# Kernel optimization log

Measured on AMD Instinct MI355X. Metric: run time of the kernel, lower is better.

## Reference

```python
import jax, jax.numpy as jnp
import numpy as np

N_ENT = 50000
N_REL = 500
N_EDGE = 800000
H_DIM = 96
BN_EPS = 1e-5


def setup_inputs() -> dict:
    key = jax.random.key(0)
    k1, k2, k3, k4, k5 = jax.random.split(key, 5)
    return {
        "ent_emb": jax.random.normal(k1, (N_ENT, H_DIM), dtype=jnp.float32),
        "rel_emb": jax.random.normal(k2, (N_REL, H_DIM), dtype=jnp.float32),
        "neigh_w": jax.random.normal(k3, (H_DIM, H_DIM), dtype=jnp.float32) * (1.0 / np.sqrt(H_DIM)),
        "bn_gamma": jnp.ones((H_DIM,), dtype=jnp.float32),
        "bn_beta": jnp.zeros((H_DIM,), dtype=jnp.float32),
        "rel_id": jax.random.randint(k4, (N_EDGE,), 0, N_REL, dtype=jnp.int64),
        "dst": jax.random.randint(k5, (N_EDGE,), 0, N_ENT, dtype=jnp.int64),
    }


def reference(ent_emb, rel_emb, neigh_w, bn_gamma, bn_beta, rel_id, dst):
    n_nodes = ent_emb.shape[0]
    # per-edge gather: edge feature = relation embedding  [E, D]
    e = rel_emb[rel_id]
    # e_dot_v: dot of edge feature with destination node embedding  [E]
    score = jnp.sum(e * ent_emb[dst], axis=-1)
    # edge softmax over incoming edges of each destination node
    seg_max = jax.ops.segment_max(score, dst, num_segments=n_nodes)  # [N]
    w = jnp.exp(score - seg_max[dst])                                # [E]
    seg_sum = jax.ops.segment_sum(w, dst, num_segments=n_nodes)      # [N]
    alpha = w / seg_sum[dst]                                         # [E]
    # weighted scatter-sum aggregation into destination nodes  [N, D]
    neigh = jax.ops.segment_sum(e * alpha[:, None], dst, num_segments=n_nodes)
    # linear
    out = neigh @ neigh_w
    # BatchNorm1d (training mode: batch stats over nodes, biased var)
    mu = jnp.mean(out, axis=0)
    var = jnp.mean((out - mu) ** 2, axis=0)
    out = (out - mu) * jax.lax.rsqrt(var + BN_EPS) * bn_gamma + bn_beta
    return jnp.tanh(out)
```

## Files before the change

### kernel.cpp

```cpp
#include <hip/hip_runtime.h>
#include <math.h>

#define N_ENT   50000
#define N_REL   500
#define N_EDGE  800000
#define H       96
#define BN_EPS  1e-5f
#define DEG_CAP 64

#define RELW_BLOCKS ((N_REL * H + 255) / 256)
#define ZERO_N      (N_ENT + 2 * H)
#define ZERO_BLOCKS ((ZERO_N + 255) / 256)

__global__ __launch_bounds__(256) void k_init(
        const float* __restrict__ rel, const float* __restrict__ W,
        float* __restrict__ relW, unsigned* __restrict__ zbase) {
    if (blockIdx.x < RELW_BLOCKS) {
        __shared__ float Ws[H * H];
        for (int i = threadIdx.x; i < H * H; i += 256) Ws[i] = W[i];
        __syncthreads();
        int t = blockIdx.x * 256 + threadIdx.x;
        if (t >= N_REL * H) return;
        int r = t / H;
        int c = t - r * H;
        const float4* rr = (const float4*)(rel + (size_t)r * H);
        float acc = 0.0f;
#pragma unroll
        for (int i = 0; i < H / 4; ++i) {
            float4 a = rr[i];
            acc += a.x * Ws[(4 * i + 0) * H + c];
            acc += a.y * Ws[(4 * i + 1) * H + c];
            acc += a.z * Ws[(4 * i + 2) * H + c];
            acc += a.w * Ws[(4 * i + 3) * H + c];
        }
        relW[t] = acc;
    } else {
        int i = (blockIdx.x - RELW_BLOCKS) * 256 + threadIdx.x;
        if (i < ZERO_N) zbase[i] = 0u;
    }
}

__global__ __launch_bounds__(256) void k_bucket(
        const int* __restrict__ dst, const int* __restrict__ rel_id,
        int* __restrict__ cursor, unsigned short* __restrict__ pay) {
    int e = blockIdx.x * 256 + threadIdx.x;
    if (e >= N_EDGE) return;
    int d = dst[e];
    int r = rel_id[e];
    int p = atomicAdd(cursor + d, 1);
    if (p < DEG_CAP) pay[d * DEG_CAP + p] = (unsigned short)r;
}

__global__ __launch_bounds__(256) void k_node(
        const float* __restrict__ ent, const float* __restrict__ rel,
        const unsigned short* __restrict__ pay, const int* __restrict__ cursor,
        const float* __restrict__ relW, float* __restrict__ out) {
    __shared__ float sh_w[4][DEG_CAP];
    __shared__ int   sh_r[4][DEG_CAP];
    int wv   = threadIdx.x >> 6;
    int lane = threadIdx.x & 63;
    int n = blockIdx.x * 4 + wv;
    if (n >= N_ENT) return;
    int cnt = min(cursor[n], DEG_CAP);

    {
        int q  = lane & 3;
        int jj = lane >> 2;
        const float4* er = (const float4*)(ent + (size_t)n * H) + q * 6;
        float4 e0 = er[0], e1 = er[1], e2 = er[2], e3 = er[3], e4 = er[4], e5 = er[5];
        int npass = (cnt + 15) >> 4;
        for (int p = 0; p < npass; ++p) {
            int j = (p << 4) + jj;
            bool valid = (j < cnt);
            int rid = valid ? (int)pay[n * DEG_CAP + j] : 0;
            float part = 0.0f;
            if (valid) {
                const float4* rr = (const float4*)(rel + (size_t)rid * H) + q * 6;
                float4 b;
                b = rr[0]; part += e0.x*b.x + e0.y*b.y + e0.z*b.z + e0.w*b.w;
                b = rr[1]; part += e1.x*b.x + e1.y*b.y + e1.z*b.z + e1.w*b.w;
                b = rr[2]; part += e2.x*b.x + e2.y*b.y + e2.z*b.z + e2.w*b.w;
                b = rr[3]; part += e3.x*b.x + e3.y*b.y + e3.z*b.z + e3.w*b.w;
                b = rr[4]; part += e4.x*b.x + e4.y*b.y + e4.z*b.z + e4.w*b.w;
                b = rr[5]; part += e5.x*b.x + e5.y*b.y + e5.z*b.z + e5.w*b.w;
            }
            part += __shfl_xor(part, 1);
            part += __shfl_xor(part, 2);
            if (valid && q == 0) { sh_w[wv][j] = part; sh_r[wv][j] = rid; }
        }
    }

    {
        float sc = (lane < cnt) ? sh_w[wv][lane] : -INFINITY;
        float m = sc;
#pragma unroll
        for (int off = 1; off < 64; off <<= 1)
            m = fmaxf(m, __shfl_xor(m, off));
        float w = (lane < cnt) ? __expf(sc - m) : 0.0f;
        float s = w;
#pragma unroll
        for (int off = 1; off < 64; off <<= 1)
            s += __shfl_xor(s, off);
        float inv = (cnt > 0) ? 1.0f / s : 0.0f;
        if (lane < cnt) sh_w[wv][lane] = w * inv;
    }

    int g  = lane & 7;
    int es = lane >> 3;
    float4 a0 = make_float4(0.f, 0.f, 0.f, 0.f);
    float4 a1 = make_float4(0.f, 0.f, 0.f, 0.f);
    float4 a2 = make_float4(0.f, 0.f, 0.f, 0.f);
    for (int k = es; k < cnt; k += 8) {
        float w  = sh_w[wv][k];
        int rid  = sh_r[wv][k];
        const float4* p = (const float4*)(relW + (size_t)rid * H + g * 12);
        float4 f0 = p[0], f1 = p[1], f2 = p[2];
        a0.x += w * f0.x; a0.y += w * f0.y; a0.z += w * f0.z; a0.w += w * f0.w;
        a1.x += w * f1.x; a1.y += w * f1.y; a1.z += w * f1.z; a1.w += w * f1.w;
        a2.x += w * f2.x; a2.y += w * f2.y; a2.z += w * f2.z; a2.w += w * f2.w;
    }
#pragma unroll
    for (int off = 8; off < 64; off <<= 1) {
        a0.x += __shfl_xor(a0.x, off); a0.y += __shfl_xor(a0.y, off);
        a0.z += __shfl_xor(a0.z, off); a0.w += __shfl_xor(a0.w, off);
        a1.x += __shfl_xor(a1.x, off); a1.y += __shfl_xor(a1.y, off);
        a1.z += __shfl_xor(a1.z, off); a1.w += __shfl_xor(a1.w, off);
        a2.x += __shfl_xor(a2.x, off); a2.y += __shfl_xor(a2.y, off);
        a2.z += __shfl_xor(a2.z, off); a2.w += __shfl_xor(a2.w, off);
    }
    if (es == 0) {
        float4* op = (float4*)(out + (size_t)n * H + g * 12);
        op[0] = a0; op[1] = a1; op[2] = a2;
    }
}

__global__ __launch_bounds__(256) void k_bnstats(
        const float* __restrict__ out, float* __restrict__ bn_sum,
        float* __restrict__ bn_sumsq) {
    __shared__ float sh_s[4][H], sh_q[4][H];
    int wave = threadIdx.x >> 6;
    int lane = threadIdx.x & 63;
    float4 s = make_float4(0.f, 0.f, 0.f, 0.f);
    float4 ss = make_float4(0.f, 0.f, 0.f, 0.f);
    if (lane < H / 4) {
        for (int n = blockIdx.x * 4 + wave; n < N_ENT; n += gridDim.x * 4) {
            float4 v = ((const float4*)(out + (size_t)n * H))[lane];
            s.x += v.x; s.y += v.y; s.z += v.z; s.w += v.w;
            ss.x += v.x * v.x; ss.y += v.y * v.y;
            ss.z += v.z * v.z; ss.w += v.w * v.w;
        }
        ((float4*)sh_s[wave])[lane] = s;
        ((float4*)sh_q[wave])[lane] = ss;
    }
    __syncthreads();
    int d = threadIdx.x;
    if (d < H) {
        float ts = sh_s[0][d] + sh_s[1][d] + sh_s[2][d] + sh_s[3][d];
        float tq = sh_q[0][d] + sh_q[1][d] + sh_q[2][d] + sh_q[3][d];
        atomicAdd(bn_sum + d, ts);
        atomicAdd(bn_sumsq + d, tq);
    }
}

__device__ __forceinline__ float fast_tanh(float x) {
    return 1.0f - 2.0f / (__expf(2.0f * x) + 1.0f);
}

__global__ __launch_bounds__(256) void k_bnapply(
        float* __restrict__ out, const float* __restrict__ bn_sum,
        const float* __restrict__ bn_sumsq, const float* __restrict__ gamma,
        const float* __restrict__ beta) {
    int t = blockIdx.x * 256 + threadIdx.x;
    if (t >= N_ENT * H / 4) return;
    int c4 = t % (H / 4);
    const float inv_n = 1.0f / (float)N_ENT;
    float4 v = ((const float4*)out)[t];
    float4 sm = ((const float4*)bn_sum)[c4];
    float4 sq = ((const float4*)bn_sumsq)[c4];
    float4 g  = ((const float4*)gamma)[c4];
    float4 b  = ((const float4*)beta)[c4];
    float mu0 = sm.x * inv_n, mu1 = sm.y * inv_n, mu2 = sm.z * inv_n, mu3 = sm.w * inv_n;
    float r0 = rsqrtf(sq.x * inv_n - mu0 * mu0 + BN_EPS);
    float r1 = rsqrtf(sq.y * inv_n - mu1 * mu1 + BN_EPS);
    float r2 = rsqrtf(sq.z * inv_n - mu2 * mu2 + BN_EPS);
    float r3 = rsqrtf(sq.w * inv_n - mu3 * mu3 + BN_EPS);
    float4 o;
    o.x = fast_tanh((v.x - mu0) * r0 * g.x + b.x);
    o.y = fast_tanh((v.y - mu1) * r1 * g.y + b.y);
    o.z = fast_tanh((v.z - mu2) * r2 * g.z + b.z);
    o.w = fast_tanh((v.w - mu3) * r3 * g.w + b.w);
    ((float4*)out)[t] = o;
}

extern "C" void kernel_launch(void* const* d_in, const int* in_sizes, int n_in,
                              void* d_out, int out_size, void* d_ws, size_t ws_size,
                              hipStream_t stream) {
    const float* ent   = (const float*)d_in[0];
    const float* rel   = (const float*)d_in[1];
    const float* W     = (const float*)d_in[2];
    const float* gamma = (const float*)d_in[3];
    const float* beta  = (const float*)d_in[4];
    const int* rel_id  = (const int*)d_in[5];
    const int* dst     = (const int*)d_in[6];
    float* out = (float*)d_out;

    float* ws       = (float*)d_ws;
    int*   cursor   = (int*)ws;
    float* bn_sum   = ws + N_ENT;
    float* bn_sumsq = bn_sum + H;
    float* relW     = bn_sumsq + H;
    unsigned short* pay = (unsigned short*)(relW + N_REL * H);

    k_init<<<RELW_BLOCKS + ZERO_BLOCKS, 256, 0, stream>>>(
        rel, W, relW, (unsigned*)cursor);
    k_bucket<<<(N_EDGE + 255) / 256, 256, 0, stream>>>(dst, rel_id, cursor, pay);
    k_node<<<(N_ENT + 3) / 4, 256, 0, stream>>>(ent, rel, pay, cursor, relW, out);
    k_bnstats<<<784, 256, 0, stream>>>(out, bn_sum, bn_sumsq);
    k_bnapply<<<(N_ENT * H / 4 + 255) / 256, 256, 0, stream>>>(
        out, bn_sum, bn_sumsq, gamma, beta);
}
```

Baseline: 212.3 us.

## Fuse BN statistics into node kernel and keep per-edge data in registers

Removes the separate BN-stats kernel. Each node block now reduces its own outputs in shared memory and atomically adds them into one of 16 partial-sum copies, which spreads out atomic contention. Relation ids are loaded once per lane and passed by shuffle instead of through shared memory and repeated payload loads. The first 16 relW rows are prefetched before the softmax so their loads overlap with it. The apply kernel folds the 16 copies and precomputes a per-channel scale and shift. The risks are that invalid slots now read payload entries that were never written (masked afterwards), and that all 64 entries are read unconditionally.

Result: slower. 264.8 us (+24.7%).

```diff
diff --git a/kernel.cpp b/kernel.cpp
--- a/kernel.cpp
+++ b/kernel.cpp
@@ -7,9 +7,10 @@
 #define H       96
 #define BN_EPS  1e-5f
 #define DEG_CAP 64
+#define NCOPY   16
 
 #define RELW_BLOCKS ((N_REL * H + 255) / 256)
-#define ZERO_N      (N_ENT + 2 * H)
+#define ZERO_N      (N_ENT + NCOPY * 2 * H)
 #define ZERO_BLOCKS ((ZERO_N + 255) / 256)
 
 __global__ __launch_bounds__(256) void k_init(
@@ -54,14 +55,17 @@
 __global__ __launch_bounds__(256) void k_node(
         const float* __restrict__ ent, const float* __restrict__ rel,
         const unsigned short* __restrict__ pay, const int* __restrict__ cursor,
-        const float* __restrict__ relW, float* __restrict__ out) {
-    __shared__ float sh_w[4][DEG_CAP];
-    __shared__ int   sh_r[4][DEG_CAP];
+        const float* __restrict__ relW, float* __restrict__ out,
+        float* __restrict__ bn_part) {
+    __shared__ float sh_s[4][DEG_CAP];
+    __shared__ float sh_o[4][H];
     int wv   = threadIdx.x >> 6;
     int lane = threadIdx.x & 63;
     int n = blockIdx.x * 4 + wv;
-    if (n >= N_ENT) return;
     int cnt = min(cursor[n], DEG_CAP);
+
+    int myrid = (int)pay[(size_t)n * DEG_CAP + lane];
+    if (lane >= cnt) myrid = 0;
 
     {
         int q  = lane & 3;
@@ -71,27 +75,35 @@
         int npass = (cnt + 15) >> 4;
         for (int p = 0; p < npass; ++p) {
             int j = (p << 4) + jj;
+            int rid = __shfl(myrid, j);
             bool valid = (j < cnt);
-            int rid = valid ? (int)pay[n * DEG_CAP + j] : 0;
             float part = 0.0f;
-            if (valid) {
-                const float4* rr = (const float4*)(rel + (size_t)rid * H) + q * 6;
-                float4 b;
-                b = rr[0]; part += e0.x*b.x + e0.y*b.y + e0.z*b.z + e0.w*b.w;
-                b = rr[1]; part += e1.x*b.x + e1.y*b.y + e1.z*b.z + e1.w*b.w;
-                b = rr[2]; part += e2.x*b.x + e2.y*b.y + e2.z*b.z + e2.w*b.w;
-                b = rr[3]; part += e3.x*b.x + e3.y*b.y + e3.z*b.z + e3.w*b.w;
-                b = rr[4]; part += e4.x*b.x + e4.y*b.y + e4.z*b.z + e4.w*b.w;
-                b = rr[5]; part += e5.x*b.x + e5.y*b.y + e5.z*b.z + e5.w*b.w;
-            }
+            const float4* rr = (const float4*)(rel + (size_t)rid * H) + q * 6;
+            float4 b;
+            b = rr[0]; part += e0.x*b.x + e0.y*b.y + e0.z*b.z + e0.w*b.w;
+            b = rr[1]; part += e1.x*b.x + e1.y*b.y + e1.z*b.z + e1.w*b.w;
+            b = rr[2]; part += e2.x*b.x + e2.y*b.y + e2.z*b.z + e2.w*b.w;
+            b = rr[3]; part += e3.x*b.x + e3.y*b.y + e3.z*b.z + e3.w*b.w;
+            b = rr[4]; part += e4.x*b.x + e4.y*b.y + e4.z*b.z + e4.w*b.w;
+            b = rr[5]; part += e5.x*b.x + e5.y*b.y + e5.z*b.z + e5.w*b.w;
             part += __shfl_xor(part, 1);
             part += __shfl_xor(part, 2);
-            if (valid && q == 0) { sh_w[wv][j] = part; sh_r[wv][j] = rid; }
-        }
-    }
-
+            if (valid && q == 0) sh_s[wv][j] = part;
+        }
+    }
+
+    int g  = lane & 7;
+    int es = lane >> 3;
+    int rj0 = __shfl(myrid, es);
+    int rj1 = __shfl(myrid, es + 8);
+    const float4* p0 = (const float4*)(relW + (size_t)rj0 * H + g * 12);
+    const float4* p1 = (const float4*)(relW + (size_t)rj1 * H + g * 12);
+    float4 f00 = p0[0], f01 = p0[1], f02 = p0[2];
+    float4 f10 = p1[0], f11 = p1[1], f12 = p1[2];
+
+    float alpha;
     {
-        float sc = (lane < cnt) ? sh_w[wv][lane] : -INFINITY;
+        float sc = (lane < cnt) ? sh_s[wv][lane] : -INFINITY;
         float m = sc;
 #pragma unroll
         for (int off = 1; off < 64; off <<= 1)
@@ -102,17 +114,25 @@
         for (int off = 1; off < 64; off <<= 1)
             s += __shfl_xor(s, off);
         float inv = (cnt > 0) ? 1.0f / s : 0.0f;
-        if (lane < cnt) sh_w[wv][lane] = w * inv;
-    }
-
-    int g  = lane & 7;
-    int es = lane >> 3;
-    float4 a0 = make_float4(0.f, 0.f, 0.f, 0.f);
-    float4 a1 = make_float4(0.f, 0.f, 0.f, 0.f);
-    float4 a2 = make_float4(0.f, 0.f, 0.f, 0.f);
-    for (int k = es; k < cnt; k += 8) {
-        float w  = sh_w[wv][k];
-        int rid  = sh_r[wv][k];
+        alpha = w * inv;
+    }
+
+    float w0 = __shfl(alpha, es);
+    float w1 = __shfl(alpha, es + 8);
+    float4 a0, a1, a2;
+    a0.x = w0*f00.x + w1*f10.x; a0.y = w0*f00.y + w1*f10.y;
+    a0.z = w0*f00.z + w1*f10.z; a0.w = w0*f00.w + w1*f10.w;
+    a1.x = w0*f01.x + w1*f11.x; a1.y = w0*f01.y + w1*f11.y;
+    a1.z = w0*f01.z + w1*f11.z; a1.w = w0*f01.w + w1*f11.w;
+    a2.x = w0*f02.x + w1*f12.x; a2.y = w0*f02.y + w1*f12.y;
+    a2.z = w0*f02.z + w1*f12.z; a2.w = w0*f02.w + w1*f12.w;
+
+    int rem = cnt - 16;
+    int npass2 = (rem > 0) ? ((rem + 7) >> 3) : 0;
+    for (int m2 = 0; m2 < npass2; ++m2) {
+        int k = es + 16 + (m2 << 3);
+        int rid = __shfl(myrid, k);
+        float w = __shfl(alpha, k);
         const float4* p = (const float4*)(relW + (size_t)rid * H + g * 12);
         float4 f0 = p[0], f1 = p[1], f2 = p[2];
         a0.x += w * f0.x; a0.y += w * f0.y; a0.z += w * f0.z; a0.w += w * f0.w;
@@ -131,34 +151,22 @@
     if (es == 0) {
         float4* op = (float4*)(out + (size_t)n * H + g * 12);
         op[0] = a0; op[1] = a1; op[2] = a2;
-    }
-}
-
-__global__ __launch_bounds__(256) void k_bnstats(
-        const float* __restrict__ out, float* __restrict__ bn_sum,
-        float* __restrict__ bn_sumsq) {
-    __shared__ float sh_s[4][H], sh_q[4][H];
-    int wave = threadIdx.x >> 6;
-    int lane = threadIdx.x & 63;
-    float4 s = make_float4(0.f, 0.f, 0.f, 0.f);
-    float4 ss = make_float4(0.f, 0.f, 0.f, 0.f);
-    if (lane < H / 4) {
-        for (int n = blockIdx.x * 4 + wave; n < N_ENT; n += gridDim.x * 4) {
-            float4 v = ((const float4*)(out + (size_t)n * H))[lane];
-            s.x += v.x; s.y += v.y; s.z += v.z; s.w += v.w;
-            ss.x += v.x * v.x; ss.y += v.y * v.y;
-            ss.z += v.z * v.z; ss.w += v.w * v.w;
-        }
-        ((float4*)sh_s[wave])[lane] = s;
-        ((float4*)sh_q[wave])[lane] = ss;
-    }
+        float4* so = (float4*)(&sh_o[wv][g * 12]);
+        so[0] = a0; so[1] = a1; so[2] = a2;
+    }
+
     __syncthreads();
-    int d = threadIdx.x;
-    if (d < H) {
-        float ts = sh_s[0][d] + sh_s[1][d] + sh_s[2][d] + sh_s[3][d];
-        float tq = sh_q[0][d] + sh_q[1][d] + sh_q[2][d] + sh_q[3][d];
-        atomicAdd(bn_sum + d, ts);
-        atomicAdd(bn_sumsq + d, tq);
+    int t = threadIdx.x;
+    if (t < H) {
+        float s = 0.0f, qq = 0.0f;
+#pragma unroll
+        for (int w = 0; w < 4; ++w) {
+            float v = sh_o[w][t];
+            s += v; qq += v * v;
+        }
+        float* bp = bn_part + (blockIdx.x & (NCOPY - 1)) * (2 * H);
+        atomicAdd(bp + t, s);
+        atomicAdd(bp + H + t, qq);
     }
 }
 
@@ -167,29 +175,36 @@
 }
 
 __global__ __launch_bounds__(256) void k_bnapply(
-        float* __restrict__ out, const float* __restrict__ bn_sum,
-        const float* __restrict__ bn_sumsq, const float* __restrict__ gamma,
-        const float* __restrict__ beta) {
-    int t = blockIdx.x * 256 + threadIdx.x;
-    if (t >= N_ENT * H / 4) return;
-    int c4 = t % (H / 4);
-    const float inv_n = 1.0f / (float)N_ENT;
-    float4 v = ((const float4*)out)[t];
-    float4 sm = ((const float4*)bn_sum)[c4];
-    float4 sq = ((const float4*)bn_sumsq)[c4];
-    float4 g  = ((const float4*)gamma)[c4];
-    float4 b  = ((const float4*)beta)[c4];
-    float mu0 = sm.x * inv_n, mu1 = sm.y * inv_n, mu2 = sm.z * inv_n, mu3 = sm.w * inv_n;
-    float r0 = rsqrtf(sq.x * inv_n - mu0 * mu0 + BN_EPS);
-    float r1 = rsqrtf(sq.y * inv_n - mu1 * mu1 + BN_EPS);
-    float r2 = rsqrtf(sq.z * inv_n - mu2 * mu2 + BN_EPS);
-    float r3 = rsqrtf(sq.w * inv_n - mu3 * mu3 + BN_EPS);
+        float* __restrict__ out, const float* __restrict__ bn_part,
+        const float* __restrict__ gamma, const float* __restrict__ beta) {
+    __shared__ float sA[H], sB[H];
+    int t = threadIdx.x;
+    if (t < H) {
+        float s = 0.0f, qq = 0.0f;
+#pragma unroll
+        for (int c = 0; c < NCOPY; ++c) {
+            s  += bn_part[c * (2 * H) + t];
+            qq += bn_part[c * (2 * H) + H + t];
+        }
+        const float inv_n = 1.0f / (float)N_ENT;
+        float mu = s * inv_n;
+        float r  = rsqrtf(qq * inv_n - mu * mu + BN_EPS);
+        float gg = gamma[t];
+        float a  = r * gg;
+        sA[t] = a;
+        sB[t] = beta[t] - mu * a;
+    }
+    __syncthreads();
+    int idx = blockIdx.x * 256 + t;
+    if (idx >= N_ENT * H / 4) return;
+    int c4 = idx % (H / 4);
+    float4 v = ((const float4*)out)[idx];
     float4 o;
-    o.x = fast_tanh((v.x - mu0) * r0 * g.x + b.x);
-    o.y = fast_tanh((v.y - mu1) * r1 * g.y + b.y);
-    o.z = fast_tanh((v.z - mu2) * r2 * g.z + b.z);
-    o.w = fast_tanh((v.w - mu3) * r3 * g.w + b.w);
-    ((float4*)out)[t] = o;
+    o.x = fast_tanh(v.x * sA[4 * c4 + 0] + sB[4 * c4 + 0]);
+    o.y = fast_tanh(v.y * sA[4 * c4 + 1] + sB[4 * c4 + 1]);
+    o.z = fast_tanh(v.z * sA[4 * c4 + 2] + sB[4 * c4 + 2]);
+    o.w = fast_tanh(v.w * sA[4 * c4 + 3] + sB[4 * c4 + 3]);
+    ((float4*)out)[idx] = o;
 }
 
 extern "C" void kernel_launch(void* const* d_in, const int* in_sizes, int n_in,
@@ -206,16 +221,15 @@
 
     float* ws       = (float*)d_ws;
     int*   cursor   = (int*)ws;
-    float* bn_sum   = ws + N_ENT;
-    float* bn_sumsq = bn_sum + H;
-    float* relW     = bn_sumsq + H;
+    float* bn_part  = ws + N_ENT;
+    float* relW     = bn_part + NCOPY * 2 * H;
     unsigned short* pay = (unsigned short*)(relW + N_REL * H);
 
     k_init<<<RELW_BLOCKS + ZERO_BLOCKS, 256, 0, stream>>>(
         rel, W, relW, (unsigned*)cursor);
     k_bucket<<<(N_EDGE + 255) / 256, 256, 0, stream>>>(dst, rel_id, cursor, pay);
-    k_node<<<(N_ENT + 3) / 4, 256, 0, stream>>>(ent, rel, pay, cursor, relW, out);
-    k_bnstats<<<784, 256, 0, stream>>>(out, bn_sum, bn_sumsq);
+    k_node<<<(N_ENT + 3) / 4, 256, 0, stream>>>(ent, rel, pay, cursor, relW, out,
+                                                bn_part);
     k_bnapply<<<(N_ENT * H / 4 + 255) / 256, 256, 0, stream>>>(
-        out, bn_sum, bn_sumsq, gamma, beta);
-}
+        out, bn_part, gamma, beta);
+}
```
